# Kernel optimization log

Hardware: AMD Instinct MI355X
Metric: run time of the kernel (lower is better)

Reference implementation:

```python
import jax, jax.numpy as jnp
import numpy as np
from jax import lax

BZ, CAPACITY, SEQ_LEN, IN_VAR, N_EDGES = 64, 134, 288, 16, 96


def setup_inputs() -> dict:
    key = jax.random.key(0)
    ks = jax.random.split(key, 9)
    s_gcn = 1.0 / np.sqrt(SEQ_LEN)
    s_conv = 1.0 / np.sqrt(IN_VAR * 3)
    s_fc = 1.0 / np.sqrt(2 * IN_VAR)
    return {
        "src": jax.random.normal(ks[0], (BZ, CAPACITY, SEQ_LEN, IN_VAR), dtype=jnp.float32),
        "feature_edge_index": jax.random.randint(ks[1], (2, N_EDGES), 0, IN_VAR, dtype=jnp.int32),
        # SAGEConv(seq_len, seq_len): out = lin_l(mean_neighbors) + lin_r(x); lin_l has bias
        "Wl": jax.random.uniform(ks[2], (SEQ_LEN, SEQ_LEN), jnp.float32, -s_gcn, s_gcn),
        "Wr": jax.random.uniform(ks[3], (SEQ_LEN, SEQ_LEN), jnp.float32, -s_gcn, s_gcn),
        "b_gcn": jax.random.uniform(ks[4], (SEQ_LEN,), jnp.float32, -s_gcn, s_gcn),
        "conv1_w": jax.random.uniform(ks[5], (IN_VAR, IN_VAR, 3), jnp.float32, -s_conv, s_conv),
        "conv2_w": jax.random.uniform(ks[6], (IN_VAR, IN_VAR, 5), jnp.float32, -s_conv, s_conv),
        "fc_w": jax.random.uniform(ks[7], (IN_VAR, 2 * IN_VAR), jnp.float32, -s_fc, s_fc),
        "fc_b": jax.random.uniform(ks[8], (IN_VAR,), jnp.float32, -s_fc, s_fc),
    }


def reference(src, feature_edge_index, Wl, Wr, b_gcn, conv1_w, conv2_w, fc_w, fc_b):
    bz, cap, S, F = src.shape  # [bz, capacity, seq_len, in_var]
    B = bz * cap
    # node features for the feature graph: [B, in_var, seq_len]
    x2 = src.transpose(0, 1, 3, 2).reshape(B, F, S)
    e_src, e_dst = feature_edge_index[0], feature_edge_index[1]
    # SAGEConv mean aggregation over shared edge_index, vectorized across B graphs
    gathered = x2[:, e_src, :]                                   # [B, E, S]
    agg = jnp.zeros_like(x2).at[:, e_dst, :].add(gathered)       # [B, F, S]
    deg = jnp.zeros((F,), x2.dtype).at[e_dst].add(1.0)
    mean = agg / jnp.maximum(deg, 1.0)[None, :, None]
    feat = (jnp.einsum('bns,ts->bnt', mean, Wl)
            + jnp.einsum('bns,ts->bnt', x2, Wr) + b_gcn)          # [B, F, S]
    fea_fea = feat.reshape(bz, cap, F, S).transpose(0, 1, 3, 2)   # [bz,cap,S,F]
    # dual temporal Conv1d branches (same padding, no bias) on [B, F, S]
    dn = ('NCH', 'OIH', 'NCH')
    c1 = lax.conv_general_dilated(x2, conv1_w, (1,), [(1, 1)], dimension_numbers=dn)
    c2 = lax.conv_general_dilated(x2, conv2_w, (2,), [(2, 2)][:1] * 1, dimension_numbers=dn) if False else lax.conv_general_dilated(x2, conv2_w, (1,), [(2, 2)], dimension_numbers=dn)
    temporal = (c1 + c2).transpose(0, 2, 1).reshape(bz, cap, S, F)
    com = jnp.concatenate([fea_fea, temporal], axis=-1)           # [bz,cap,S,2F]
    com = jnp.einsum('bcsf,of->bcso', com, fc_w) + fc_b
    # dropout is identity in eval mode
    return src + com
```

## Files before the change

kernel.cpp:

```cpp
#include <hip/hip_runtime.h>
#include <hip/hip_bf16.h>

typedef short short8 __attribute__((ext_vector_type(8)));
typedef float float4v __attribute__((ext_vector_type(4)));
typedef unsigned short ushort4v __attribute__((ext_vector_type(4)));

#define BTOT 8576
#define SEQ 288
#define NF 16
#define SPN 296
#define XTROWS 294
#define XT_USH (XTROWS * 16)
#define XN_USH (16 * SPN)
#define PBN (XT_USH + XN_USH)
#define WCVW 104

__device__ __forceinline__ unsigned short f2b(float f) {
    union { float f; unsigned u; } v; v.f = f;
    unsigned r = v.u + 0x7FFF + ((v.u >> 16) & 1);
    return (unsigned short)(r >> 16);
}
__device__ __forceinline__ float b2f(unsigned short u) {
    union { unsigned u; float f; } v; v.u = ((unsigned)u) << 16; return v.f;
}

__global__ void wcast_kernel(const float* __restrict__ a, const float* __restrict__ b,
                             unsigned short* __restrict__ o) {
    int i = blockIdx.x * 256 + threadIdx.x;
    o[i]         = f2b(a[i]);
    o[82944 + i] = f2b(b[i]);
}

template<int WPRE>
__device__ __forceinline__ short8 ldw(const unsigned short* __restrict__ wb,
                                      const float* __restrict__ wf, int idx) {
    if (WPRE) {
        return *(const short8*)&wb[idx];
    } else {
        const float* p = &wf[idx];
        float4 w0 = *(const float4*)p, w1 = *(const float4*)(p + 4);
        short8 a;
        a[0] = (short)f2b(w0.x); a[1] = (short)f2b(w0.y);
        a[2] = (short)f2b(w0.z); a[3] = (short)f2b(w0.w);
        a[4] = (short)f2b(w1.x); a[5] = (short)f2b(w1.y);
        a[6] = (short)f2b(w1.z); a[7] = (short)f2b(w1.w);
        return a;
    }
}

#define LDB(KK9, B_) do {                                                      \
    const int s0_ = (KK9) * 32;                                                \
    (B_)[0] = *(const short8*)&xsN0[li * SPN + s0_ + 8 * g];                   \
    (B_)[1] = *(const short8*)&xsN1[li * SPN + s0_ + 8 * g];                   \
} while (0)

#define LDA(WT_, WF_, KK9, A_) do {                                            \
    const int s0_ = (KK9) * 32;                                                \
    _Pragma("unroll")                                                          \
    for (int m_ = 0; m_ < 3; ++m_)                                             \
        if (m_ < nt) (A_)[m_] = ldw<WPRE>(WT_, WF_, arow[m_] + s0_ + 8 * g);   \
} while (0)

#define MFK(A_, B_) do {                                                       \
    _Pragma("unroll")                                                          \
    for (int m_ = 0; m_ < 3; ++m_)                                             \
        if (m_ < nt) {                                                         \
            acc[m_][0] = __builtin_amdgcn_mfma_f32_16x16x32_bf16((A_)[m_], (B_)[0], acc[m_][0], 0, 0, 0); \
            acc[m_][1] = __builtin_amdgcn_mfma_f32_16x16x32_bf16((A_)[m_], (B_)[1], acc[m_][1], 0, 0, 0); \
        }                                                                      \
} while (0)

#define GEMM9(WT_, WF_) do {                                                   \
    short8 aC[3], aN[3];                                                       \
    LDA(WT_, WF_, 0, aC);                                                      \
    LDA(WT_, WF_, 1, aN);                                                      \
    _Pragma("unroll")                                                          \
    for (int kk = 0; kk < 9; ++kk) {                                           \
        short8 bb[2];                                                          \
        LDB(kk, bb);                                                           \
        if (kk & 1) { MFK(aN, bb); if (kk < 7) LDA(WT_, WF_, kk + 2, aN); }    \
        else        { MFK(aC, bb); if (kk < 7) LDA(WT_, WF_, kk + 2, aC); }    \
    }                                                                          \
} while (0)

template<int WPRE>
__global__ __launch_bounds__(512, 6) void stconv_mfma(
    const float* __restrict__ src,
    const int*   __restrict__ eidx,
    const float* __restrict__ Wlf,
    const float* __restrict__ Wrf,
    const unsigned short* __restrict__ Wbf,
    const float* __restrict__ bgcn,
    const float* __restrict__ cw1g,
    const float* __restrict__ cw2g,
    const float* __restrict__ fcwg,
    const float* __restrict__ fcbg,
    float*       __restrict__ out)
{
    __shared__ unsigned short pool[2 * PBN];
    __shared__ unsigned short wcv[16 * WCVW];
    __shared__ unsigned short fcwB[16 * 40];
    __shared__ unsigned short MB[16 * 40];
    __shared__ float bg[SEQ];
    __shared__ float Msc[256];
    __shared__ float fcb[16];

    const int tid  = threadIdx.x;
    const int wav  = tid >> 6;
    const int nb   = wav >> 2;
    const int wloc = wav & 3;
    const int lane = tid & 63;
    const int li   = lane & 15;
    const int g    = lane >> 4;
    const int b0   = blockIdx.x * 2;

    unsigned short* xsT = pool + nb * PBN;
    unsigned short* xsN = pool + nb * PBN + XT_USH;
    const float* srcb = src + (size_t)(b0 + nb) * (SEQ * NF);

    if (tid < 256) Msc[tid] = 0.0f;
    for (int i = tid; i < 16 * 40; i += 512) MB[i] = 0;
    for (int i = tid; i < 16 * WCVW; i += 512) wcv[i] = 0;
    if (tid < 192) {
        int nb2 = tid / 96, r2 = tid % 96;
        int r = r2 >> 4, f = r2 & 15;
        int row = (r < 2) ? r : 288 + r;
        pool[nb2 * PBN + row * 16 + f] = 0;
    }
    __syncthreads();

    if (tid < 96) atomicAdd(&Msc[eidx[96 + tid] * 16 + eidx[tid]], 1.0f);
    {
        const int q = tid & 255;
        #pragma unroll
        for (int i = 0; i < 5; ++i) {
            int c = i * 256 + q;
            if (c < 1152) {
                int s = c >> 2, f0 = (c & 3) << 2;
                float4 v = *(const float4*)(srcb + (c << 2));
                ushort4v h;
                h[0] = f2b(v.x); h[1] = f2b(v.y); h[2] = f2b(v.z); h[3] = f2b(v.w);
                *(ushort4v*)&xsT[(s + 2) * 16 + f0] = h;
                xsN[(f0 + 0) * SPN + s] = h[0];
                xsN[(f0 + 1) * SPN + s] = h[1];
                xsN[(f0 + 2) * SPN + s] = h[2];
                xsN[(f0 + 3) * SPN + s] = h[3];
            }
        }
    }
    for (int j = tid; j < 1280; j += 512) {
        int fo = j / 80, rem = j % 80, fi = rem / 5, d = rem % 5;
        float t = cw2g[(fo * 16 + fi) * 5 + d];
        if (d >= 1 && d <= 3) t += cw1g[(fo * 16 + fi) * 3 + (d - 1)];
        wcv[fo * WCVW + d * 16 + fi] = f2b(t);
    }
    if (tid < 512) fcwB[(tid >> 5) * 40 + (tid & 31)] = f2b(fcwg[tid]);
    if (tid < SEQ) bg[tid] = bgcn[tid];
    if (tid < 16) fcb[tid] = fcbg[tid];
    __syncthreads();

    if (tid < 16) {
        float deg = 0.0f;
        #pragma unroll
        for (int f = 0; f < 16; ++f) deg += Msc[tid * 16 + f];
        float inv = 1.0f / fmaxf(deg, 1.0f);
        #pragma unroll
        for (int f = 0; f < 16; ++f) MB[tid * 40 + f] = f2b(Msc[tid * 16 + f] * inv);
    }
    __syncthreads();

    const int t2 = (wav == 0) ? 16 : ((wav == 5) ? 17 : -1);
    const int nt = (t2 >= 0) ? 3 : 2;
    const int tts[3] = {wav, wav + 8, t2};
    const int arow[3] = {(tts[0] * 16 + li) * 288, (tts[1] * 16 + li) * 288,
                         (t2 >= 0) ? ((t2 * 16 + li) * 288) : 0};

    const unsigned short* WblT = Wbf;
    const unsigned short* WbrT = Wbf + 288 * 288;
    const unsigned short* xsN0 = pool + XT_USH;
    const unsigned short* xsN1 = pool + PBN + XT_USH;

    float4v acc[3][2];

    #pragma unroll
    for (int m = 0; m < 3; ++m)
        if (m < nt) {
            #pragma unroll
            for (int r = 0; r < 4; ++r) {
                float bv = bg[tts[m] * 16 + 4 * g + r];
                acc[m][0][r] = bv; acc[m][1][r] = bv;
            }
        }
    GEMM9(WbrT, Wrf);
    __syncthreads();

    {
        short8 bm = *(const short8*)&MB[li * 40 + 8 * g];
        unsigned short* msN = xsN;
        for (int st = wloc; st < 18; st += 4) {
            int s0 = st * 16;
            short8 a = {0, 0, 0, 0, 0, 0, 0, 0};
            if (g < 2) a = *(const short8*)&xsT[(s0 + li + 2) * 16 + 8 * g];
            float4v c = {0.f, 0.f, 0.f, 0.f};
            c = __builtin_amdgcn_mfma_f32_16x16x32_bf16(a, bm, c, 0, 0, 0);
            ushort4v p;
            #pragma unroll
            for (int r = 0; r < 4; ++r) p[r] = f2b(c[r]);
            *(ushort4v*)&msN[li * SPN + s0 + 4 * g] = p;
        }
    }
    __syncthreads();

    GEMM9(WblT, Wlf);

    ushort4v p5o[3][2];
    #pragma unroll
    for (int m = 0; m < 3; ++m)
        if (m < nt) {
            #pragma unroll
            for (int r = 0; r < 4; ++r) {
                p5o[m][0][r] = f2b(acc[m][0][r]);
                p5o[m][1][r] = f2b(acc[m][1][r]);
            }
        }

    ushort4v p6o[5];
    {
        short8 cb0 = *(const short8*)&wcv[li * WCVW + 0  + 8 * g];
        short8 cb1 = *(const short8*)&wcv[li * WCVW + 32 + 8 * g];
        short8 cb2 = *(const short8*)&wcv[li * WCVW + 64 + 8 * g];
        const int fi0   = (g & 1) * 8;
        const int dbase = g >> 1;
        #pragma unroll
        for (int it = 0; it < 5; ++it) {
            int st = wloc + 4 * it;
            if (st < 18) {
                int s0 = st * 16;
                int rbase = (s0 + li + dbase) * 16 + fi0;
                short8 a0 = *(const short8*)&xsT[rbase];
                short8 a1 = *(const short8*)&xsT[rbase + 32];
                short8 a2 = *(const short8*)&xsT[rbase + 64];
                float4v c = {0.f, 0.f, 0.f, 0.f};
                c = __builtin_amdgcn_mfma_f32_16x16x32_bf16(a0, cb0, c, 0, 0, 0);
                c = __builtin_amdgcn_mfma_f32_16x16x32_bf16(a1, cb1, c, 0, 0, 0);
                c = __builtin_amdgcn_mfma_f32_16x16x32_bf16(a2, cb2, c, 0, 0, 0);
                #pragma unroll
                for (int r = 0; r < 4; ++r) p6o[it][r] = f2b(c[r]);
            }
        }
    }

    ushort4v res16[5];
    #pragma unroll
    for (int it = 0; it < 5; ++it) {
        int st = wloc + 4 * it;
        if (st < 18) {
            int s0 = st * 16;
            #pragma unroll
            for (int r = 0; r < 4; ++r)
                res16[it][r] = xsT[(s0 + 4 * g + r + 2) * 16 + li];
        }
    }
    __syncthreads();

    {
        unsigned short* cat0 = pool;
        unsigned short* cat1 = pool + PBN;
        #pragma unroll
        for (int m = 0; m < 3; ++m)
            if (m < nt) {
                #pragma unroll
                for (int r = 0; r < 4; ++r) {
                    int pos = tts[m] * 16 + 4 * g + r;
                    cat0[pos * 32 + li] = p5o[m][0][r];
                    cat1[pos * 32 + li] = p5o[m][1][r];
                }
            }
        unsigned short* catb = pool + nb * PBN;
        #pragma unroll
        for (int it = 0; it < 5; ++it) {
            int st = wloc + 4 * it;
            if (st < 18) {
                int s0 = st * 16;
                #pragma unroll
                for (int r = 0; r < 4; ++r)
                    catb[(s0 + 4 * g + r) * 32 + 16 + li] = p6o[it][r];
            }
        }
    }
    __syncthreads();

    {
        const unsigned short* catb = pool + nb * PBN;
        short8 fb = *(const short8*)&fcwB[li * 40 + 8 * g];
        float* outb = out + (size_t)(b0 + nb) * (SEQ * NF);
        #pragma unroll
        for (int it = 0; it < 5; ++it) {
            int st = wloc + 4 * it;
            if (st < 18) {
                int s0 = st * 16;
                float4v c;
                #pragma unroll
                for (int r = 0; r < 4; ++r) c[r] = b2f(res16[it][r]) + fcb[li];
                short8 a = *(const short8*)&catb[(s0 + li) * 32 + 8 * g];
                c = __builtin_amdgcn_mfma_f32_16x16x32_bf16(a, fb, c, 0, 0, 0);
                #pragma unroll
                for (int r = 0; r < 4; ++r) outb[(s0 + 4 * g + r) * 16 + li] = c[r];
            }
        }
    }
}

extern "C" void kernel_launch(void* const* d_in, const int* in_sizes, int n_in,
                              void* d_out, int out_size, void* d_ws, size_t ws_size,
                              hipStream_t stream)
{
    const float* src  = (const float*)d_in[0];
    const int*   eidx = (const int*)  d_in[1];
    const float* Wl   = (const float*)d_in[2];
    const float* Wr   = (const float*)d_in[3];
    const float* bgcn = (const float*)d_in[4];
    const float* cw1  = (const float*)d_in[5];
    const float* cw2  = (const float*)d_in[6];
    const float* fcw  = (const float*)d_in[7];
    const float* fcb  = (const float*)d_in[8];
    float* out = (float*)d_out;

    const size_t wbytes = (size_t)2 * 288 * 288 * sizeof(unsigned short);
    if (ws_size >= wbytes) {
        wcast_kernel<<<dim3(324), dim3(256), 0, stream>>>(Wl, Wr, (unsigned short*)d_ws);
        stconv_mfma<1><<<dim3(BTOT / 2), dim3(512), 0, stream>>>(
            src, eidx, Wl, Wr, (const unsigned short*)d_ws,
            bgcn, cw1, cw2, fcw, fcb, out);
    } else {
        stconv_mfma<0><<<dim3(BTOT / 2), dim3(512), 0, stream>>>(
            src, eidx, Wl, Wr, nullptr,
            bgcn, cw1, cw2, fcw, fcb, out);
    }
}
```

Baseline: 159.0 us.

## Prefetch B fragments, raise MFMA wave priority, and swizzle concat LDS buffer

```diff
diff --git a/kernel.cpp b/kernel.cpp
--- a/kernel.cpp
+++ b/kernel.cpp
@@ -22,6 +22,10 @@
 }
 __device__ __forceinline__ float b2f(unsigned short u) {
     union { unsigned u; float f; } v; v.u = ((unsigned)u) << 16; return v.f;
+}
+
+__device__ __forceinline__ int cat_widx(int pos, int c) {
+    return pos * 32 + ((((c >> 3) ^ ((pos >> 1) & 3)) << 3) | (c & 7));
 }
 
 __global__ void wcast_kernel(const float* __restrict__ a, const float* __restrict__ b,
@@ -62,24 +66,29 @@
 } while (0)
 
 #define MFK(A_, B_) do {                                                       \
+    __builtin_amdgcn_s_setprio(1);                                             \
     _Pragma("unroll")                                                          \
     for (int m_ = 0; m_ < 3; ++m_)                                             \
         if (m_ < nt) {                                                         \
             acc[m_][0] = __builtin_amdgcn_mfma_f32_16x16x32_bf16((A_)[m_], (B_)[0], acc[m_][0], 0, 0, 0); \
             acc[m_][1] = __builtin_amdgcn_mfma_f32_16x16x32_bf16((A_)[m_], (B_)[1], acc[m_][1], 0, 0, 0); \
         }                                                                      \
+    __builtin_amdgcn_s_setprio(0);                                             \
 } while (0)
 
 #define GEMM9(WT_, WF_) do {                                                   \
-    short8 aC[3], aN[3];                                                       \
-    LDA(WT_, WF_, 0, aC);                                                      \
-    LDA(WT_, WF_, 1, aN);                                                      \
+    short8 aC[3], aN[3], bC[2], bN[2];                                         \
+    LDA(WT_, WF_, 0, aC);  LDB(0, bC);                                         \
+    LDA(WT_, WF_, 1, aN);  LDB(1, bN);                                         \
     _Pragma("unroll")                                                          \
     for (int kk = 0; kk < 9; ++kk) {                                           \
-        short8 bb[2];                                                          \
-        LDB(kk, bb);                                                           \
-        if (kk & 1) { MFK(aN, bb); if (kk < 7) LDA(WT_, WF_, kk + 2, aN); }    \
-        else        { MFK(aC, bb); if (kk < 7) LDA(WT_, WF_, kk + 2, aC); }    \
+        if (kk & 1) {                                                          \
+            MFK(aN, bN);                                                       \
+            if (kk < 7) { LDA(WT_, WF_, kk + 2, aN); LDB(kk + 2, bN); }        \
+        } else {                                                               \
+            MFK(aC, bC);                                                       \
+            if (kk < 7) { LDA(WT_, WF_, kk + 2, aC); LDB(kk + 2, bC); }        \
+        }                                                                      \
     }                                                                          \
 } while (0)
 
@@ -241,9 +250,11 @@
                 short8 a1 = *(const short8*)&xsT[rbase + 32];
                 short8 a2 = *(const short8*)&xsT[rbase + 64];
                 float4v c = {0.f, 0.f, 0.f, 0.f};
+                __builtin_amdgcn_s_setprio(1);
                 c = __builtin_amdgcn_mfma_f32_16x16x32_bf16(a0, cb0, c, 0, 0, 0);
                 c = __builtin_amdgcn_mfma_f32_16x16x32_bf16(a1, cb1, c, 0, 0, 0);
                 c = __builtin_amdgcn_mfma_f32_16x16x32_bf16(a2, cb2, c, 0, 0, 0);
+                __builtin_amdgcn_s_setprio(0);
                 #pragma unroll
                 for (int r = 0; r < 4; ++r) p6o[it][r] = f2b(c[r]);
             }
@@ -272,8 +283,8 @@
                 #pragma unroll
                 for (int r = 0; r < 4; ++r) {
                     int pos = tts[m] * 16 + 4 * g + r;
-                    cat0[pos * 32 + li] = p5o[m][0][r];
-                    cat1[pos * 32 + li] = p5o[m][1][r];
+                    cat0[cat_widx(pos, li)] = p5o[m][0][r];
+                    cat1[cat_widx(pos, li)] = p5o[m][1][r];
                 }
             }
         unsigned short* catb = pool + nb * PBN;
@@ -284,7 +295,7 @@
                 int s0 = st * 16;
                 #pragma unroll
                 for (int r = 0; r < 4; ++r)
-                    catb[(s0 + 4 * g + r) * 32 + 16 + li] = p6o[it][r];
+                    catb[cat_widx(s0 + 4 * g + r, 16 + li)] = p6o[it][r];
             }
         }
     }
@@ -302,7 +313,8 @@
                 float4v c;
                 #pragma unroll
                 for (int r = 0; r < 4; ++r) c[r] = b2f(res16[it][r]) + fcb[li];
-                short8 a = *(const short8*)&catb[(s0 + li) * 32 + 8 * g];
+                int pos = s0 + li;
+                short8 a = *(const short8*)&catb[pos * 32 + ((g ^ ((pos >> 1) & 3)) << 3)];
                 c = __builtin_amdgcn_mfma_f32_16x16x32_bf16(a, fb, c, 0, 0, 0);
                 #pragma unroll
                 for (int r = 0; r < 4; ++r) outb[(s0 + 4 * g + r) * 16 + li] = c[r];
```

Result: slower. 198.1 us (+24.6%).
